# Performance work log

Measured on AMD Instinct MI355X. Metric: run time of the kernel, lower is better.

## Reference

```python
import jax, jax.numpy as jnp
import numpy as np
from jax import lax

E = 300      # _embsize
H = 32       # attention heads
ADIM = 64    # projection_dim (attention and values dim)
FF = 100     # feedforward hidden dim
NK = 11      # gaussian kernels
NCONV = 5    # conv kernel sizes 1..5
COUT = 16    # conv out channels for k>=2

def _kernel_mus(n):
    l = [1.0]
    b = 2.0 / (n - 1)
    l.append(1 - b / 2)
    for i in range(1, n - 1):
        l.append(l[i] - b)
    return l

def _kernel_sigmas(n):
    b = 2.0 / (n - 1)
    return [0.0001] + [0.5 * b] * (n - 1)

MU = jnp.asarray(_kernel_mus(NK), jnp.float32).reshape(1, 1, 1, 1, NK)
SIG = jnp.asarray(_kernel_sigmas(NK), jnp.float32).reshape(1, 1, 1, 1, NK)

def _pos_features(T, d):
    # allennlp add_positional_features, min_timescale=1, max_timescale=1e4, d even
    nt = d // 2
    inv = np.exp(np.arange(nt, dtype=np.float32) * -(np.log(1e4) / (nt - 1)))
    pos = np.arange(T, dtype=np.float32)[:, None] * inv[None, :]
    return jnp.asarray(np.concatenate([np.sin(pos), np.cos(pos)], axis=1))

def _layer_norm(x, g, b, eps=1e-6):
    m = jnp.mean(x, -1, keepdims=True)
    s = jnp.std(x, -1, keepdims=True)  # biased std, as allennlp LayerNorm
    return g * (x - m) / (s + eps) + b

def _mhsa(x, mask, Wc, bc, Wo, bo):
    # allennlp MultiHeadSelfAttention: combined projection, scale=sqrt(input_dim//heads)
    B, T, _ = x.shape
    comb = x @ Wc + bc                                   # [B,T,3*ADIM]
    q, k, v = comb[..., :ADIM], comb[..., ADIM:2 * ADIM], comb[..., 2 * ADIM:]
    dh = ADIM // H
    split = lambda t: t.reshape(B, T, H, dh).transpose(0, 2, 1, 3)
    q, k, v = split(q), split(k), split(v)
    scale = float(np.sqrt(E // H))
    sim = jnp.einsum('bhqd,bhkd->bhqk', q / scale, k)
    m = mask[:, None, None, :]
    p = jax.nn.softmax(sim * m, axis=-1) * m             # old allennlp masked_softmax
    p = p / (jnp.sum(p, -1, keepdims=True) + 1e-13)
    o = jnp.einsum('bhqk,bhkd->bhqd', p, v).transpose(0, 2, 1, 3).reshape(B, T, ADIM)
    return o @ Wo + bo

def _encode(x, mask, W1, b1, W2, b2, ffg, ffb, Wc, bc, Wo, bo, lng, lnb):
    # StackedSelfAttentionEncoder, 1 layer, all dropouts = 0
    out = x + _pos_features(x.shape[1], E)[None]
    ff = jax.nn.relu(out @ W1 + b1) @ W2 + b2
    ff = _layer_norm(ff + out, ffg, ffb)                 # residual (dims match)
    att = _mhsa(ff, mask, Wc, bc, Wo, bo)
    return _layer_norm(att + ff, lng, lnb)

def _conv(x, w, b, k):
    if k > 1:
        x = jnp.pad(x, ((0, 0), (0, 0), (0, k - 1), (0, k - 1)))  # ConstantPad2d(0,k-1,0,k-1)
    y = lax.conv_general_dilated(x, w, (1, 1), 'VALID',
                                 dimension_numbers=('NCHW', 'OIHW', 'NCHW'))
    y = y + b[None, :, None, None]
    if k > 1:
        y = jnp.max(y, axis=1, keepdims=True)            # MaxPool3d over channel dim
    return y

def setup_inputs() -> dict:
    key = jax.random.key(0)
    ks = iter(jax.random.split(key, 40))
    B, Q, D = 16, 32, 512
    nrm = lambda shape, s=0.05: jax.random.normal(next(ks), shape, jnp.float32) * s
    return {
        'query_embeddings': jax.random.normal(next(ks), (B, Q, E), jnp.float32),
        'document_embeddings': jax.random.normal(next(ks), (B, D, E), jnp.float32),
        'query_pad_oov_mask': jnp.ones((B, Q), jnp.float32),
        'document_pad_oov_mask': jnp.ones((B, D), jnp.float32),
        'query_idfs': jax.random.uniform(next(ks), (B, Q, 1), jnp.float32),
        'document_idfs': jax.random.uniform(next(ks), (B, D, 1), jnp.float32),
        'W1': nrm((E, FF)), 'b1': jnp.zeros((FF,), jnp.float32),
        'W2': nrm((FF, E)), 'b2': jnp.zeros((E,), jnp.float32),
        'ffg': jnp.ones((E,), jnp.float32), 'ffb': jnp.zeros((E,), jnp.float32),
        'Wc': nrm((E, 3 * ADIM)), 'bc': jnp.zeros((3 * ADIM,), jnp.float32),
        'Wo': nrm((ADIM, E)), 'bo': jnp.zeros((E,), jnp.float32),
        'lng': jnp.ones((E,), jnp.float32), 'lnb': jnp.zeros((E,), jnp.float32),
        'c1w': nrm((1, 2, 1, 1)), 'c1b': jnp.zeros((1,), jnp.float32),
        'c2w': nrm((COUT, 2, 2, 2)), 'c2b': jnp.zeros((COUT,), jnp.float32),
        'c3w': nrm((COUT, 2, 3, 3)), 'c3b': jnp.zeros((COUT,), jnp.float32),
        'c4w': nrm((COUT, 2, 4, 4)), 'c4b': jnp.zeros((COUT,), jnp.float32),
        'c5w': nrm((COUT, 2, 5, 5)), 'c5b': jnp.zeros((COUT,), jnp.float32),
        'dw': nrm((1, NK * NCONV)), 'db': jnp.zeros((1,), jnp.float32),
        'dmw': nrm((1, NK * NCONV)), 'dmb': jnp.zeros((1,), jnp.float32),
        'cw': nrm((1, 2)),
    }

def reference(query_embeddings, document_embeddings, query_pad_oov_mask,
              document_pad_oov_mask, query_idfs, document_idfs,
              W1, b1, W2, b2, ffg, ffb, Wc, bc, Wo, bo, lng, lnb,
              c1w, c1b, c2w, c2b, c3w, c3b, c4w, c4b, c5w, c5b,
              dw, db, dmw, dmb, cw):
    qm, dmask = query_pad_oov_mask, document_pad_oov_mask
    enc = lambda x, m: _encode(x, m, W1, b1, W2, b2, ffg, ffb, Wc, bc, Wo, bo, lng, lnb)
    q_ctx = enc(query_embeddings, qm) * qm[..., None]
    d_ctx = enc(document_embeddings, dmask) * dmask[..., None]
    # cosine on raw embeddings, dot product on contextualized
    qn = query_embeddings / (jnp.linalg.norm(query_embeddings, axis=-1, keepdims=True) + 1e-13)
    dn = document_embeddings / (jnp.linalg.norm(document_embeddings, axis=-1, keepdims=True) + 1e-13)
    cos = jnp.einsum('bqe,bde->bqd', qn, dn)[:, None]
    dot = jnp.einsum('bqe,bde->bqd', q_ctx, d_ctx)[:, None]
    combined = jnp.tanh(jnp.concatenate([cos, dot], axis=1))     # [B,2,Q,D]
    convs = [_conv(combined, w, b, k) for k, (w, b) in enumerate(
        [(c1w, c1b), (c2w, c2b), (c3w, c3b), (c4w, c4b), (c5w, c5b)], start=1)]
    all_conv = jnp.concatenate(convs, axis=1)[..., None]         # [B,5,Q,D,1]
    qd_mask = (qm[:, :, None] * dmask[:, None, :])[:, None, :, :, None]  # [B,1,Q,D,1]
    raw = jnp.exp(-(all_conv - MU) ** 2 / (2.0 * SIG ** 2))      # [B,5,Q,D,NK]
    masked = raw * qd_mask
    doc_len = jnp.sum(dmask, 1)                                  # [B]
    pkq = jnp.sum(masked, axis=3)                                # [B,5,Q,NK]
    log_pkq = jnp.log(jnp.clip(pkq, 1e-10, None)) * qm[:, None, :, None]
    per_kernel = jnp.sum(log_pkq, axis=2)                        # [B,5,NK]
    pkq_mean = pkq / doc_len[:, None, None, None]
    log_pkq_mean = jnp.log(jnp.clip(pkq_mean, 1e-10, None)) * qm[:, None, :, None]
    per_kernel_mean = jnp.sum(log_pkq_mean, axis=2)
    B = per_kernel.shape[0]
    d1 = per_kernel.reshape(B, -1) @ dw.T + db
    d2 = per_kernel_mean.reshape(B, -1) @ dmw.T + dmb
    return (jnp.concatenate([d1, d2], axis=1) @ cw.T)[:, 0]
```

## Files before the change

### kernel.cpp

```cpp
#include <hip/hip_runtime.h>

namespace {

constexpr int E_  = 300;
constexpr int FF_ = 100;
constexpr int AD_ = 64;
constexpr int NH_ = 32;
constexpr int CD_ = 192;
constexpr int B_  = 16;
constexpr int TQ_ = 32;
constexpr int TD_ = 512;
constexpr int NK_ = 11;
constexpr int DOCBLK_ = 512;

__device__ __forceinline__ float wave_sum(float v) {
#pragma unroll
  for (int o = 32; o > 0; o >>= 1) v += __shfl_down(v, o);
  return v;
}

__device__ __forceinline__ int swz16(int e, int t) {
  return e * 16 + (t ^ (((e >> 2) & 7) << 1));
}

__device__ __forceinline__ void fma4(float4& a, float s, const float4& w) {
  a.x = fmaf(s, w.x, a.x); a.y = fmaf(s, w.y, a.y);
  a.z = fmaf(s, w.z, a.z); a.w = fmaf(s, w.w, a.w);
}

__device__ __forceinline__ void gl_lds16(const float4* g, float4* l) {
  __builtin_amdgcn_global_load_lds(
      (const __attribute__((address_space(1))) void*)g,
      (__attribute__((address_space(3))) void*)l, 16, 0, 0);
}

__device__ __forceinline__ void stage_chunk(const float4* __restrict__ src,
                                            float4* __restrict__ dst,
                                            int n, int tid) {
  for (int j = tid; j < n; j += 256) gl_lds16(src + j, dst + j);
}

__global__ __launch_bounds__(256)
void encode_front_v5(const float* __restrict__ qe, const float* __restrict__ de,
                     const float* __restrict__ W1, const float* __restrict__ b1,
                     const float* __restrict__ W2, const float* __restrict__ b2,
                     const float* __restrict__ ffg, const float* __restrict__ ffb,
                     const float* __restrict__ Wc, const float* __restrict__ bc,
                     float* __restrict__ ffq, float* __restrict__ combq,
                     float* __restrict__ qn,
                     float* __restrict__ ffd, float* __restrict__ combd,
                     float* __restrict__ dnT)
{
  __shared__ float  s_A[4800];
  __shared__ float  s_h1[1600];
  __shared__ float4 s_w[2][1500];
  __shared__ float  s_stat[16][17];
  __shared__ float  s_norm[16];

  const int tid = threadIdx.x;
  const int ct = tid & 31, tg = tid >> 5;
  const int t0 = tg * 2;
  const bool doc = (blockIdx.x < DOCBLK_);
  const int sb = doc ? blockIdx.x : (blockIdx.x - DOCBLK_);
  const float* xs = (doc ? de : qe) + (size_t)sb * 16 * E_;
  float* ffo = doc ? ffd : ffq;
  float* cmo = doc ? combd : combq;
  const size_t tok0 = (size_t)sb * 16;
  const int bb_ = doc ? (int)(tok0 >> 9) : (int)(tok0 >> 5);
  const int tp0 = doc ? (int)(tok0 & 511) : (int)(tok0 & 31);

  const float4* W1f4 = (const float4*)W1;
  const float4* W2f4 = (const float4*)W2;
  const float4* Wcf4 = (const float4*)Wc;

  stage_chunk(W1f4, &s_w[0][0], 1500, tid);

  for (int i = tid; i < 1200; i += 256) {
    const float4 v = *(const float4*)(xs + (size_t)i * 4);
    const int t = i / 75, e0 = (i % 75) * 4;
    s_A[swz16(e0 + 0, t)] = v.x; s_A[swz16(e0 + 1, t)] = v.y;
    s_A[swz16(e0 + 2, t)] = v.z; s_A[swz16(e0 + 3, t)] = v.w;
  }
  __syncthreads();
  {
    const int tk = tid & 15, ch = tid >> 4;
    const int kb = ch * 19, ke = (kb + 19 < 300) ? kb + 19 : 300;
    float ss = 0.f;
    for (int k = kb; k < ke; ++k) { const float v = s_A[swz16(k, tk)]; ss = fmaf(v, v, ss); }
    s_stat[ch][tk] = ss;
  }
  __syncthreads();
  if (tid < 16) {
    float s = 0.f;
#pragma unroll
    for (int i = 0; i < 16; ++i) s += s_stat[i][tid];
    s_norm[tid] = 1.f / (sqrtf(s) + 1e-13f);
  }
  __syncthreads();
  for (int i = tid; i < 1200; i += 256) {
    const int t = i / 75, e0 = (i % 75) * 4;
    const int tp = tp0 + t;
    const float nm = s_norm[t];
#pragma unroll
    for (int j = 0; j < 4; ++j) {
      const int e = e0 + j;
      const int slot = swz16(e, t);
      const float raw = s_A[slot];
      if (doc) dnT[((size_t)bb_ * E_ + e) * 512 + tp] = raw * nm;
      else     qn[(tok0 + t) * E_ + e] = raw * nm;
      const int f = (e < 150) ? e : e - 150;
      const float ang = __expf(-0.061814365f * (float)f) * (float)tp;
      s_A[slot] = raw + ((e < 150) ? sinf(ang) : cosf(ang));
    }
  }
  __syncthreads();

  {
    const int cq = (ct < 25) ? ct : 24;
    float4 a1[2];
    a1[0] = make_float4(0.f, 0.f, 0.f, 0.f);
    a1[1] = make_float4(0.f, 0.f, 0.f, 0.f);
    for (int c = 0; c < 5; ++c) {
      if (c < 4) stage_chunk(W1f4 + 1500 * (c + 1), &s_w[(c + 1) & 1][0], 1500, tid);
      else       stage_chunk(W2f4,                  &s_w[1][0],           1500, tid);
      const float4* wb = &s_w[c & 1][0];
#pragma unroll 6
      for (int kk = 0; kk < 60; ++kk) {
        const float2 xv = *(const float2*)&s_A[swz16(c * 60 + kk, t0)];
        const float4 w = wb[kk * 25 + cq];
        fma4(a1[0], xv.x, w); fma4(a1[1], xv.y, w);
      }
      if (c == 4 && ct < 25) {
        const float4 bb = *(const float4*)&b1[4 * ct];
#pragma unroll
        for (int r = 0; r < 2; ++r) {
          const int t = t0 + r;
          const float4 a = (r == 0) ? a1[0] : a1[1];
          s_h1[swz16(4 * ct + 0, t)] = fmaxf(a.x + bb.x, 0.f);
          s_h1[swz16(4 * ct + 1, t)] = fmaxf(a.y + bb.y, 0.f);
          s_h1[swz16(4 * ct + 2, t)] = fmaxf(a.z + bb.z, 0.f);
          s_h1[swz16(4 * ct + 3, t)] = fmaxf(a.w + bb.w, 0.f);
        }
      }
      __syncthreads();
    }
  }

  {
    const int q2 = (ct < 11) ? ct + 64 : 74;
    const bool val2 = (ct < 11);
    float4 a2[3][2];
#pragma unroll
    for (int p = 0; p < 3; ++p)
#pragma unroll
      for (int r = 0; r < 2; ++r) a2[p][r] = make_float4(0.f, 0.f, 0.f, 0.f);
    for (int c = 0; c < 5; ++c) {
      if (c < 4) stage_chunk(W2f4 + 1500 * (c + 1), &s_w[c & 1][0], 1500, tid);
      else       stage_chunk(Wcf4,                  &s_w[0][0],     1440, tid);
      const float4* wb = &s_w[(c + 1) & 1][0];
#pragma unroll 5
      for (int kk = 0; kk < 20; ++kk) {
        const float2 hv = *(const float2*)&s_h1[swz16(c * 20 + kk, t0)];
        const float4 w0 = wb[kk * 75 + ct];
        const float4 w1 = wb[kk * 75 + ct + 32];
        const float4 w2 = wb[kk * 75 + q2];
        fma4(a2[0][0], hv.x, w0); fma4(a2[0][1], hv.y, w0);
        fma4(a2[1][0], hv.x, w1); fma4(a2[1][1], hv.y, w1);
        fma4(a2[2][0], hv.x, w2); fma4(a2[2][1], hv.y, w2);
      }
      if (c == 4) {
        float sum[2] = {0.f, 0.f}, sq[2] = {0.f, 0.f};
#pragma unroll
        for (int p = 0; p < 3; ++p) {
          const int qq = (p == 0) ? ct : (p == 1) ? ct + 32 : q2;
          const bool ok = (p < 2) || val2;
          if (!ok) break;
          const float4 bb = *(const float4*)&b2[4 * qq];
#pragma unroll
          for (int r = 0; r < 2; ++r) {
            const int t = t0 + r;
            float4 v = a2[p][r];
            v.x += bb.x + s_A[swz16(4 * qq + 0, t)];
            v.y += bb.y + s_A[swz16(4 * qq + 1, t)];
            v.z += bb.z + s_A[swz16(4 * qq + 2, t)];
            v.w += bb.w + s_A[swz16(4 * qq + 3, t)];
            a2[p][r] = v;
            sum[r] += v.x + v.y + v.z + v.w;
            sq[r] = fmaf(v.x, v.x, fmaf(v.y, v.y, fmaf(v.z, v.z, fmaf(v.w, v.w, sq[r]))));
          }
        }
#pragma unroll
        for (int m = 1; m <= 16; m <<= 1) {
#pragma unroll
          for (int r = 0; r < 2; ++r) {
            sum[r] += __shfl_xor(sum[r], m);
            sq[r]  += __shfl_xor(sq[r], m);
          }
        }
#pragma unroll
        for (int r = 0; r < 2; ++r) {
          const int t = t0 + r;
          const float mean = sum[r] * (1.f / 300.f);
          const float var  = fmaxf(sq[r] * (1.f / 300.f) - mean * mean, 0.f);
          const float rstd = 1.f / (sqrtf(var) + 1e-6f);
#pragma unroll
          for (int p = 0; p < 3; ++p) {
            if (p == 2 && !val2) break;
            const int qq = (p == 0) ? ct : (p == 1) ? ct + 32 : q2;
            const int c0 = 4 * qq;
            const float4 g4 = *(const float4*)&ffg[c0];
            const float4 b4 = *(const float4*)&ffb[c0];
            const float4 v = a2[p][r];
            float4 fv;
            fv.x = fmaf(g4.x, (v.x - mean) * rstd, b4.x);
            fv.y = fmaf(g4.y, (v.y - mean) * rstd, b4.y);
            fv.z = fmaf(g4.z, (v.z - mean) * rstd, b4.z);
            fv.w = fmaf(g4.w, (v.w - mean) * rstd, b4.w);
            *(float4*)&ffo[(tok0 + t) * E_ + c0] = fv;
            s_A[swz16(c0 + 0, t)] = fv.x; s_A[swz16(c0 + 1, t)] = fv.y;
            s_A[swz16(c0 + 2, t)] = fv.z; s_A[swz16(c0 + 3, t)] = fv.w;
          }
        }
      }
      __syncthreads();
    }
  }

  {
    const int q3 = (ct < 16) ? ct + 32 : 47;
    float4 a3[2][2];
#pragma unroll
    for (int p = 0; p < 2; ++p)
#pragma unroll
      for (int r = 0; r < 2; ++r) a3[p][r] = make_float4(0.f, 0.f, 0.f, 0.f);
    for (int c = 0; c < 10; ++c) {
      if (c < 9) stage_chunk(Wcf4 + 1440 * (c + 1), &s_w[(c + 1) & 1][0], 1440, tid);
      const float4* wb = &s_w[c & 1][0];
#pragma unroll 6
      for (int kk = 0; kk < 30; ++kk) {
        const float2 xv = *(const float2*)&s_A[swz16(c * 30 + kk, t0)];
        const float4 w0 = wb[kk * 48 + ct];
        const float4 w1 = wb[kk * 48 + q3];
        fma4(a3[0][0], xv.x, w0); fma4(a3[0][1], xv.y, w0);
        fma4(a3[1][0], xv.x, w1); fma4(a3[1][1], xv.y, w1);
      }
      if (c < 9) __syncthreads();
    }
    const float4 bb0 = *(const float4*)&bc[4 * ct];
#pragma unroll
    for (int r = 0; r < 2; ++r) {
      float4 o = a3[0][r];
      o.x += bb0.x; o.y += bb0.y; o.z += bb0.z; o.w += bb0.w;
      *(float4*)&cmo[(tok0 + t0 + r) * CD_ + 4 * ct] = o;
    }
    if (ct < 16) {
      const float4 bb1 = *(const float4*)&bc[4 * (ct + 32)];
#pragma unroll
      for (int r = 0; r < 2; ++r) {
        float4 o = a3[1][r];
        o.x += bb1.x; o.y += bb1.y; o.z += bb1.z; o.w += bb1.w;
        *(float4*)&cmo[(tok0 + t0 + r) * CD_ + 4 * (ct + 32)] = o;
      }
    }
  }
}

template <int T>
__global__ __launch_bounds__(512)
void attn(const float* __restrict__ comb, const float* __restrict__ mask,
          float* __restrict__ o)
{
  __shared__ float4 s_kv[T];
  __shared__ float  s_m[T];
  const int bh = blockIdx.x, b = bh / NH_, h = bh % NH_;
  const int tid = threadIdx.x;
  const float* cb = comb + (size_t)b * T * CD_;
  if (tid < T) {
    const float* c = cb + (size_t)tid * CD_;
    const float m = mask[b * T + tid];
    s_kv[tid] = make_float4(c[AD_ + 2 * h] * m, c[AD_ + 2 * h + 1] * m,
                            c[2 * AD_ + 2 * h], c[2 * AD_ + 2 * h + 1]);
    s_m[tid] = m;
  }
  __syncthreads();
  if (tid < T) {
    const float* c = cb + (size_t)tid * CD_;
    const float q0 = c[2 * h] * (1.f / 3.f);
    const float q1 = c[2 * h + 1] * (1.f / 3.f);
    float M = -1e30f;
    for (int j = 0; j < T; ++j) {
      const float4 kv = s_kv[j];
      M = fmaxf(M, fmaf(q0, kv.x, q1 * kv.y));
    }
    float S = 0.f, W = 0.f, a0 = 0.f, a1 = 0.f;
    for (int j = 0; j < T; ++j) {
      const float4 kv = s_kv[j];
      const float s = fmaf(q0, kv.x, q1 * kv.y);
      const float z = __expf(s - M);
      const float w = z * s_m[j];
      S += z; W += w;
      a0 = fmaf(w, kv.z, a0);
      a1 = fmaf(w, kv.w, a1);
    }
    const float dn = 1.f / (W + 1e-13f * S);
    float* op = o + (size_t)(b * T + tid) * AD_ + 2 * h;
    op[0] = a0 * dn;
    op[1] = a1 * dn;
  }
}

__global__ __launch_bounds__(256)
void encode_back_v3(const float* __restrict__ oq, const float* __restrict__ od,
                    const float* __restrict__ ffq, const float* __restrict__ ffd,
                    const float* __restrict__ Wo, const float* __restrict__ bo,
                    const float* __restrict__ lng, const float* __restrict__ lnb,
                    const float* __restrict__ qm, const float* __restrict__ dm,
                    float* __restrict__ qctx, float* __restrict__ dctxT)
{
  __shared__ float  s_O[1024];
  __shared__ float4 s_w[2][1200];

  const int tid = threadIdx.x;
  const int ct = tid & 31, tg = tid >> 5;
  const int t0 = tg * 2;
  const bool doc = (blockIdx.x < DOCBLK_);
  const int sb = doc ? blockIdx.x : (blockIdx.x - DOCBLK_);
  const size_t tok0 = (size_t)sb * 16;
  const float* op = doc ? od : oq;
  const float* ffp = doc ? ffd : ffq;
  const float* mp = doc ? dm : qm;
  const int bb_ = doc ? (int)(tok0 >> 9) : 0;
  const int tp0 = doc ? (int)(tok0 & 511) : 0;

  const float4* Wof4 = (const float4*)Wo;
  stage_chunk(Wof4, &s_w[0][0], 1200, tid);

  {
    const int t = tid >> 4, c0 = (tid & 15) * 4;
    const float4 v = *(const float4*)(op + (tok0 + t) * AD_ + c0);
    s_O[swz16(c0 + 0, t)] = v.x; s_O[swz16(c0 + 1, t)] = v.y;
    s_O[swz16(c0 + 2, t)] = v.z; s_O[swz16(c0 + 3, t)] = v.w;
  }
  __syncthreads();

  const int q2 = (ct < 11) ? ct + 64 : 74;
  const bool val2 = (ct < 11);
  float4 a[3][2];
#pragma unroll
  for (int p = 0; p < 3; ++p)
#pragma unroll
    for (int r = 0; r < 2; ++r) a[p][r] = make_float4(0.f, 0.f, 0.f, 0.f);
  for (int c = 0; c < 4; ++c) {
    if (c < 3) stage_chunk(Wof4 + 1200 * (c + 1), &s_w[(c + 1) & 1][0], 1200, tid);
    const float4* wb = &s_w[c & 1][0];
#pragma unroll 4
    for (int kk = 0; kk < 16; ++kk) {
      const float2 ov = *(const float2*)&s_O[swz16(c * 16 + kk, t0)];
      const float4 w0 = wb[kk * 75 + ct];
      const float4 w1 = wb[kk * 75 + ct + 32];
      const float4 w2 = wb[kk * 75 + q2];
      fma4(a[0][0], ov.x, w0); fma4(a[0][1], ov.y, w0);
      fma4(a[1][0], ov.x, w1); fma4(a[1][1], ov.y, w1);
      fma4(a[2][0], ov.x, w2); fma4(a[2][1], ov.y, w2);
    }
    if (c < 3) __syncthreads();
  }
  float sum[2] = {0.f, 0.f}, sq[2] = {0.f, 0.f};
#pragma unroll
  for (int p = 0; p < 3; ++p) {
    const int qq = (p == 0) ? ct : (p == 1) ? ct + 32 : q2;
    const bool ok = (p < 2) || val2;
    if (!ok) break;
    const float4 bb = *(const float4*)&bo[4 * qq];
#pragma unroll
    for (int r = 0; r < 2; ++r) {
      const int t = t0 + r;
      const float4 f4 = *(const float4*)(ffp + (tok0 + t) * E_ + 4 * qq);
      float4 v = a[p][r];
      v.x += bb.x + f4.x; v.y += bb.y + f4.y;
      v.z += bb.z + f4.z; v.w += bb.w + f4.w;
      a[p][r] = v;
      sum[r] += v.x + v.y + v.z + v.w;
      sq[r] = fmaf(v.x, v.x, fmaf(v.y, v.y, fmaf(v.z, v.z, fmaf(v.w, v.w, sq[r]))));
    }
  }
#pragma unroll
  for (int m = 1; m <= 16; m <<= 1) {
#pragma unroll
    for (int r = 0; r < 2; ++r) {
      sum[r] += __shfl_xor(sum[r], m);
      sq[r]  += __shfl_xor(sq[r], m);
    }
  }
#pragma unroll
  for (int r = 0; r < 2; ++r) {
    const int t = t0 + r;
    const float mean = sum[r] * (1.f / 300.f);
    const float var  = fmaxf(sq[r] * (1.f / 300.f) - mean * mean, 0.f);
    const float rstd = 1.f / (sqrtf(var) + 1e-6f);
    const float mk = mp[tok0 + t];
#pragma unroll
    for (int p = 0; p < 3; ++p) {
      if (p == 2 && !val2) break;
      const int qq = (p == 0) ? ct : (p == 1) ? ct + 32 : q2;
      const int c0 = 4 * qq;
      const float4 g4 = *(const float4*)&lng[c0];
      const float4 b4 = *(const float4*)&lnb[c0];
      const float4 v = a[p][r];
      float4 fv;
      fv.x = fmaf(g4.x, (v.x - mean) * rstd, b4.x) * mk;
      fv.y = fmaf(g4.y, (v.y - mean) * rstd, b4.y) * mk;
      fv.z = fmaf(g4.z, (v.z - mean) * rstd, b4.z) * mk;
      fv.w = fmaf(g4.w, (v.w - mean) * rstd, b4.w) * mk;
      if (doc) {
        const int tp = tp0 + t;
        dctxT[((size_t)bb_ * E_ + c0 + 0) * 512 + tp] = fv.x;
        dctxT[((size_t)bb_ * E_ + c0 + 1) * 512 + tp] = fv.y;
        dctxT[((size_t)bb_ * E_ + c0 + 2) * 512 + tp] = fv.z;
        dctxT[((size_t)bb_ * E_ + c0 + 3) * 512 + tp] = fv.w;
      } else {
        *(float4*)&qctx[(tok0 + t) * E_ + c0] = fv;
      }
    }
  }
}

__global__ __launch_bounds__(512)
void simtanh_v2(const float* __restrict__ qctx, const float* __restrict__ qn,
                const float* __restrict__ dctxT, const float* __restrict__ dnT,
                float* __restrict__ combined)
{
  __shared__ float s_q[2 * 16 * 304];
  __shared__ float s_part[8 * 32 * 64];

  const int bid = blockIdx.x;
  const int sub = bid & 15, b = bid >> 4;
  const int qh = sub >> 3, dc = sub & 7;
  const int tid = threadIdx.x;
  const int ep = tid >> 6, dlane = tid & 63;
  const int d = dc * 64 + dlane;

  const float* qc  = qctx + ((size_t)b * 32 + qh * 16) * E_;
  const float* qnp = qn   + ((size_t)b * 32 + qh * 16) * E_;
  for (int i = tid; i < 1200; i += 512) {
    const int q = i / 75, e0 = (i % 75) * 4;
    *(float4*)&s_q[(0 * 16 + q) * 304 + e0] = *(const float4*)(qc + q * E_ + e0);
    *(float4*)&s_q[(1 * 16 + q) * 304 + e0] = *(const float4*)(qnp + q * E_ + e0);
  }
  __syncthreads();

  const float* dct = dctxT + (size_t)b * E_ * 512 + d;
  const float* dnt = dnT   + (size_t)b * E_ * 512 + d;
  float accD[16], accC[16];
#pragma unroll
  for (int q = 0; q < 16; ++q) { accD[q] = 0.f; accC[q] = 0.f; }
  const int es = ep * 40, ee = (es + 40 < 300) ? es + 40 : 300;
  for (int e0 = es; e0 < ee; e0 += 4) {
    const float dv0 = dct[(size_t)(e0 + 0) * 512];
    const float dv1 = dct[(size_t)(e0 + 1) * 512];
    const float dv2 = dct[(size_t)(e0 + 2) * 512];
    const float dv3 = dct[(size_t)(e0 + 3) * 512];
    const float dn0 = dnt[(size_t)(e0 + 0) * 512];
    const float dn1 = dnt[(size_t)(e0 + 1) * 512];
    const float dn2 = dnt[(size_t)(e0 + 2) * 512];
    const float dn3 = dnt[(size_t)(e0 + 3) * 512];
#pragma unroll
    for (int q = 0; q < 16; ++q) {
      const float4 qd = *(const float4*)&s_q[(0 * 16 + q) * 304 + e0];
      const float4 qc4 = *(const float4*)&s_q[(1 * 16 + q) * 304 + e0];
      float aD = accD[q], aC = accC[q];
      aD = fmaf(qd.x, dv0, aD); aD = fmaf(qd.y, dv1, aD);
      aD = fmaf(qd.z, dv2, aD); aD = fmaf(qd.w, dv3, aD);
      aC = fmaf(qc4.x, dn0, aC); aC = fmaf(qc4.y, dn1, aC);
      aC = fmaf(qc4.z, dn2, aC); aC = fmaf(qc4.w, dn3, aC);
      accD[q] = aD; accC[q] = aC;
    }
  }
#pragma unroll
  for (int q = 0; q < 16; ++q) {
    s_part[(ep * 32 + q * 2 + 0) * 64 + dlane] = accC[q];
    s_part[(ep * 32 + q * 2 + 1) * 64 + dlane] = accD[q];
  }
  __syncthreads();
  const int s0 = (tid >> 6) * 4;
#pragma unroll
  for (int si = 0; si < 4; ++si) {
    const int s = s0 + si;
    float v = 0.f;
#pragma unroll
    for (int p = 0; p < 8; ++p) v += s_part[(p * 32 + s) * 64 + dlane];
    const int q = s >> 1, typ = s & 1;
    combined[(((size_t)b * 2 + typ) * 32 + qh * 16 + q) * 512 + d] = tanhf(v);
  }
}

template <int K>
__device__ __forceinline__ float conv_max16(const float* __restrict__ s_in, int j,
                                            const float* __restrict__ w,
                                            const float* __restrict__ bias)
{
  float patch[2][K][K];
#pragma unroll
  for (int c = 0; c < 2; ++c)
#pragma unroll
    for (int di = 0; di < K; ++di)
#pragma unroll
      for (int dj = 0; dj < K; ++dj)
        patch[c][di][dj] = s_in[(c * 5 + di) * 516 + j + dj];
  float best = -1e30f;
#pragma unroll
  for (int oc = 0; oc < 16; ++oc) {
    float acc = bias[oc];
#pragma unroll
    for (int c = 0; c < 2; ++c)
#pragma unroll
      for (int di = 0; di < K; ++di)
#pragma unroll
        for (int dj = 0; dj < K; ++dj)
          acc = fmaf(patch[c][di][dj], w[((oc * 2 + c) * K + di) * K + dj], acc);
    best = fmaxf(best, acc);
  }
  return best;
}

__global__ __launch_bounds__(512)
void conv_all(const float* __restrict__ combined,
              const float* __restrict__ c1w, const float* __restrict__ c1b,
              const float* __restrict__ c2w, const float* __restrict__ c2b,
              const float* __restrict__ c3w, const float* __restrict__ c3b,
              const float* __restrict__ c4w, const float* __restrict__ c4b,
              const float* __restrict__ c5w, const float* __restrict__ c5b,
              float* __restrict__ convout)
{
  __shared__ float s_in[2 * 5 * 516];
  __shared__ float s_w[1730];
  __shared__ float s_b[66];
  const int blk = blockIdx.x, b = blk >> 5, i = blk & 31;
  const int tid = threadIdx.x;
  for (int idx = tid; idx < 2 * 5 * 516; idx += 512) {
    const int c = idx / (5 * 516), rem = idx % (5 * 516), r = rem / 516, j = rem % 516;
    const int row = i + r;
    float v = 0.f;
    if (row < 32 && j < 512)
      v = combined[((size_t)(b * 2 + c) * 32 + row) * 512 + j];
    s_in[idx] = v;
  }
  if (tid < 2)   s_w[tid] = c1w[tid];
  if (tid < 128) s_w[2 + tid] = c2w[tid];
  if (tid < 288) s_w[130 + tid] = c3w[tid];
  s_w[418 + tid] = c4w[tid];
  for (int idx = tid; idx < 800; idx += 512) s_w[930 + idx] = c5w[idx];
  if (tid == 0) s_b[0] = c1b[0];
  if (tid < 16) {
    s_b[1 + tid]  = c2b[tid];
    s_b[17 + tid] = c3b[tid];
    s_b[33 + tid] = c4b[tid];
    s_b[49 + tid] = c5b[tid];
  }
  __syncthreads();
  const int j = tid;
  const float o1 = fmaf(s_in[j], s_w[0], fmaf(s_in[5 * 516 + j], s_w[1], s_b[0]));
  convout[((size_t)(b * 5 + 0) * 32 + i) * 512 + j] = o1;
  convout[((size_t)(b * 5 + 1) * 32 + i) * 512 + j] = conv_max16<2>(s_in, j, s_w + 2,   s_b + 1);
  convout[((size_t)(b * 5 + 2) * 32 + i) * 512 + j] = conv_max16<3>(s_in, j, s_w + 130, s_b + 17);
  convout[((size_t)(b * 5 + 3) * 32 + i) * 512 + j] = conv_max16<4>(s_in, j, s_w + 418, s_b + 33);
  convout[((size_t)(b * 5 + 4) * 32 + i) * 512 + j] = conv_max16<5>(s_in, j, s_w + 930, s_b + 49);
}

__global__ __launch_bounds__(512)
void rbf_pkq(const float* __restrict__ convout, const float* __restrict__ dmask,
             const float* __restrict__ qmask, float* __restrict__ pkq)
{
  __shared__ float red[8][NK_];
  const int id = blockIdx.x;
  const int q = id & 31;
  const int b = id / 160;
  const int tid = threadIdx.x;
  const float x = convout[(size_t)id * 512 + tid];
  const float dmv = dmask[b * 512 + tid];
  const float mu[NK_]  = {1.f, .9f, .7f, .5f, .3f, .1f, -.1f, -.3f, -.5f, -.7f, -.9f};
  const float nis[NK_] = {-5e7f, -50.f, -50.f, -50.f, -50.f, -50.f,
                          -50.f, -50.f, -50.f, -50.f, -50.f};
  const int lane = tid & 63, w = tid >> 6;
#pragma unroll
  for (int k = 0; k < NK_; ++k) {
    const float df = x - mu[k];
    float v = __expf(df * df * nis[k]) * dmv;
    v = wave_sum(v);
    if (lane == 0) red[w][k] = v;
  }
  __syncthreads();
  if (tid < NK_) {
    float s = 0.f;
#pragma unroll
    for (int ww = 0; ww < 8; ++ww) s += red[ww][tid];
    pkq[(size_t)id * NK_ + tid] = s * qmask[b * 32 + q];
  }
}

__global__ __launch_bounds__(64)
void final_k(const float* __restrict__ pkq, const float* __restrict__ qmask,
             const float* __restrict__ dmask,
             const float* __restrict__ dw, const float* __restrict__ db,
             const float* __restrict__ dmw, const float* __restrict__ dmb,
             const float* __restrict__ cw, float* __restrict__ out)
{
  const int b = blockIdx.x, tid = threadIdx.x;
  float dl = 0.f;
  for (int j = tid; j < 512; j += 64) dl += dmask[b * 512 + j];
  dl = wave_sum(dl);
  dl = __shfl(dl, 0);
  float v1 = 0.f, v2 = 0.f;
  if (tid < 55) {
    const int c = tid / NK_, k = tid % NK_;
    const float rdl = 1.f / dl;
    float s1 = 0.f, s2 = 0.f;
    for (int q = 0; q < 32; ++q) {
      const float p = pkq[(size_t)((b * 5 + c) * 32 + q) * NK_ + k];
      const float qmv = qmask[b * 32 + q];
      s1 += logf(fmaxf(p, 1e-10f)) * qmv;
      s2 += logf(fmaxf(p * rdl, 1e-10f)) * qmv;
    }
    v1 = s1 * dw[tid];
    v2 = s2 * dmw[tid];
  }
  v1 = wave_sum(v1);
  v2 = wave_sum(v2);
  if (tid == 0) out[b] = (v1 + db[0]) * cw[0] + (v2 + dmb[0]) * cw[1];
}

}

extern "C" void kernel_launch(void* const* d_in, const int* in_sizes, int n_in,
                              void* d_out, int out_size, void* d_ws, size_t ws_size,
                              hipStream_t stream)
{
  const float* qe  = (const float*)d_in[0];
  const float* de  = (const float*)d_in[1];
  const float* qm  = (const float*)d_in[2];
  const float* dm  = (const float*)d_in[3];
  const float* W1  = (const float*)d_in[6];
  const float* b1  = (const float*)d_in[7];
  const float* W2  = (const float*)d_in[8];
  const float* b2  = (const float*)d_in[9];
  const float* ffg = (const float*)d_in[10];
  const float* ffb = (const float*)d_in[11];
  const float* Wc  = (const float*)d_in[12];
  const float* bc  = (const float*)d_in[13];
  const float* Wo  = (const float*)d_in[14];
  const float* bo  = (const float*)d_in[15];
  const float* lng = (const float*)d_in[16];
  const float* lnb = (const float*)d_in[17];
  const float* c1w = (const float*)d_in[18];
  const float* c1b = (const float*)d_in[19];
  const float* c2w = (const float*)d_in[20];
  const float* c2b = (const float*)d_in[21];
  const float* c3w = (const float*)d_in[22];
  const float* c3b = (const float*)d_in[23];
  const float* c4w = (const float*)d_in[24];
  const float* c4b = (const float*)d_in[25];
  const float* c5w = (const float*)d_in[26];
  const float* c5b = (const float*)d_in[27];
  const float* dwp  = (const float*)d_in[28];
  const float* dbp  = (const float*)d_in[29];
  const float* dmwp = (const float*)d_in[30];
  const float* dmbp = (const float*)d_in[31];
  const float* cwp  = (const float*)d_in[32];

  float* ws = (float*)d_ws;
  size_t off = 0;
  auto alloc = [&](size_t n) { float* p = ws + off; off += n; return p; };
  float* ffq      = alloc((size_t)B_ * TQ_ * E_);
  float* combq    = alloc((size_t)B_ * TQ_ * CD_);
  float* oq       = alloc((size_t)B_ * TQ_ * AD_);
  float* qctx     = alloc((size_t)B_ * TQ_ * E_);
  float* qn       = alloc((size_t)B_ * TQ_ * E_);
  float* ffd      = alloc((size_t)B_ * TD_ * E_);
  float* combd    = alloc((size_t)B_ * TD_ * CD_);
  float* od       = alloc((size_t)B_ * TD_ * AD_);
  float* dctxT    = alloc((size_t)B_ * E_ * TD_);
  float* dnT      = alloc((size_t)B_ * E_ * TD_);
  float* combined = alloc((size_t)B_ * 2 * TQ_ * TD_);
  float* convout  = alloc((size_t)B_ * 5 * TQ_ * TD_);
  float* pkq      = alloc((size_t)B_ * 5 * TQ_ * NK_);

  encode_front_v5<<<DOCBLK_ + 32, 256, 0, stream>>>(
      qe, de, W1, b1, W2, b2, ffg, ffb, Wc, bc,
      ffq, combq, qn, ffd, combd, dnT);
  attn<TQ_><<<B_ * NH_, 64, 0, stream>>>(combq, qm, oq);
  attn<TD_><<<B_ * NH_, 512, 0, stream>>>(combd, dm, od);
  encode_back_v3<<<DOCBLK_ + 32, 256, 0, stream>>>(
      oq, od, ffq, ffd, Wo, bo, lng, lnb, qm, dm, qctx, dctxT);
  simtanh_v2<<<256, 512, 0, stream>>>(qctx, qn, dctxT, dnT, combined);
  conv_all<<<B_ * 32, 512, 0, stream>>>(
      combined, c1w, c1b, c2w, c2b, c3w, c3b, c4w, c4b, c5w, c5b, convout);
  rbf_pkq<<<B_ * 5 * TQ_, 512, 0, stream>>>(convout, dm, qm, pkq);
  final_k<<<B_, 64, 0, stream>>>(pkq, qm, dm, dwp, dbp, dmwp, dmbp, cwp,
                                 (float*)d_out);
}
```

Measured before the change: 382.0 us.

## Fuse conv and RBF pooling; stage weights via registers with single LDS buffer

The conv kernel now computes the gaussian kernel pooling directly on its five conv outputs. This removes the convout intermediate buffer (B*5*Q*D floats) and the separate rbf_pkq launch. Separately, the encoder kernels drop the async global_load_lds double buffer. They instead prefetch the next weight chunk into registers, commit it to a single LDS buffer and add a barrier per chunk, which halves weight LDS use but adds register pressure and extra synchronisation.

```diff
diff --git a/kernel.cpp b/kernel.cpp
--- a/kernel.cpp
+++ b/kernel.cpp
@@ -28,20 +28,8 @@
   a.z = fmaf(s, w.z, a.z); a.w = fmaf(s, w.w, a.w);
 }
 
-__device__ __forceinline__ void gl_lds16(const float4* g, float4* l) {
-  __builtin_amdgcn_global_load_lds(
-      (const __attribute__((address_space(1))) void*)g,
-      (__attribute__((address_space(3))) void*)l, 16, 0, 0);
-}
-
-__device__ __forceinline__ void stage_chunk(const float4* __restrict__ src,
-                                            float4* __restrict__ dst,
-                                            int n, int tid) {
-  for (int j = tid; j < n; j += 256) gl_lds16(src + j, dst + j);
-}
-
 __global__ __launch_bounds__(256)
-void encode_front_v5(const float* __restrict__ qe, const float* __restrict__ de,
+void encode_front_v8(const float* __restrict__ qe, const float* __restrict__ de,
                      const float* __restrict__ W1, const float* __restrict__ b1,
                      const float* __restrict__ W2, const float* __restrict__ b2,
                      const float* __restrict__ ffg, const float* __restrict__ ffb,
@@ -53,7 +41,7 @@
 {
   __shared__ float  s_A[4800];
   __shared__ float  s_h1[1600];
-  __shared__ float4 s_w[2][1500];
+  __shared__ float4 s_w4[1500];
   __shared__ float  s_stat[16][17];
   __shared__ float  s_norm[16];
 
@@ -73,7 +61,16 @@
   const float4* W2f4 = (const float4*)W2;
   const float4* Wcf4 = (const float4*)Wc;
 
-  stage_chunk(W1f4, &s_w[0][0], 1500, tid);
+  float4 r0, r1, r2, r3, r4, r5;
+#define LOADC(srcp, n) { const float4* _s = (srcp); \
+    r0 = _s[tid]; r1 = _s[tid + 256]; r2 = _s[tid + 512]; \
+    r3 = _s[tid + 768]; r4 = _s[tid + 1024]; \
+    if (tid + 1280 < (n)) r5 = _s[tid + 1280]; }
+#define COMMITC(n) { s_w4[tid] = r0; s_w4[tid + 256] = r1; s_w4[tid + 512] = r2; \
+    s_w4[tid + 768] = r3; s_w4[tid + 1024] = r4; \
+    if (tid + 1280 < (n)) s_w4[tid + 1280] = r5; }
+
+  LOADC(W1f4, 1500);
 
   for (int i = tid; i < 1200; i += 256) {
     const float4 v = *(const float4*)(xs + (size_t)i * 4);
@@ -121,21 +118,22 @@
     a1[0] = make_float4(0.f, 0.f, 0.f, 0.f);
     a1[1] = make_float4(0.f, 0.f, 0.f, 0.f);
     for (int c = 0; c < 5; ++c) {
-      if (c < 4) stage_chunk(W1f4 + 1500 * (c + 1), &s_w[(c + 1) & 1][0], 1500, tid);
-      else       stage_chunk(W2f4,                  &s_w[1][0],           1500, tid);
-      const float4* wb = &s_w[c & 1][0];
+      COMMITC(1500);
+      __syncthreads();
+      if (c < 4) LOADC(W1f4 + 1500 * (c + 1), 1500)
+      else       LOADC(W2f4, 1500)
 #pragma unroll 6
       for (int kk = 0; kk < 60; ++kk) {
         const float2 xv = *(const float2*)&s_A[swz16(c * 60 + kk, t0)];
-        const float4 w = wb[kk * 25 + cq];
+        const float4 w = s_w4[kk * 25 + cq];
         fma4(a1[0], xv.x, w); fma4(a1[1], xv.y, w);
       }
       if (c == 4 && ct < 25) {
         const float4 bb = *(const float4*)&b1[4 * ct];
 #pragma unroll
-        for (int r = 0; r < 2; ++r) {
-          const int t = t0 + r;
-          const float4 a = (r == 0) ? a1[0] : a1[1];
+        for (int rr = 0; rr < 2; ++rr) {
+          const int t = t0 + rr;
+          const float4 a = (rr == 0) ? a1[0] : a1[1];
           s_h1[swz16(4 * ct + 0, t)] = fmaxf(a.x + bb.x, 0.f);
           s_h1[swz16(4 * ct + 1, t)] = fmaxf(a.y + bb.y, 0.f);
           s_h1[swz16(4 * ct + 2, t)] = fmaxf(a.z + bb.z, 0.f);
@@ -153,17 +151,18 @@
 #pragma unroll
     for (int p = 0; p < 3; ++p)
 #pragma unroll
-      for (int r = 0; r < 2; ++r) a2[p][r] = make_float4(0.f, 0.f, 0.f, 0.f);
+      for (int rr = 0; rr < 2; ++rr) a2[p][rr] = make_float4(0.f, 0.f, 0.f, 0.f);
     for (int c = 0; c < 5; ++c) {
-      if (c < 4) stage_chunk(W2f4 + 1500 * (c + 1), &s_w[c & 1][0], 1500, tid);
-      else       stage_chunk(Wcf4,                  &s_w[0][0],     1440, tid);
-      const float4* wb = &s_w[(c + 1) & 1][0];
+      COMMITC(1500);
+      __syncthreads();
+      if (c < 4) LOADC(W2f4 + 1500 * (c + 1), 1500)
+      else       LOADC(Wcf4, 1440)
 #pragma unroll 5
       for (int kk = 0; kk < 20; ++kk) {
         const float2 hv = *(const float2*)&s_h1[swz16(c * 20 + kk, t0)];
-        const float4 w0 = wb[kk * 75 + ct];
-        const float4 w1 = wb[kk * 75 + ct + 32];
-        const float4 w2 = wb[kk * 75 + q2];
+        const float4 w0 = s_w4[kk * 75 + ct];
+        const float4 w1 = s_w4[kk * 75 + ct + 32];
+        const float4 w2 = s_w4[kk * 75 + q2];
         fma4(a2[0][0], hv.x, w0); fma4(a2[0][1], hv.y, w0);
         fma4(a2[1][0], hv.x, w1); fma4(a2[1][1], hv.y, w1);
         fma4(a2[2][0], hv.x, w2); fma4(a2[2][1], hv.y, w2);
@@ -177,31 +176,31 @@
           if (!ok) break;
           const float4 bb = *(const float4*)&b2[4 * qq];
 #pragma unroll
-          for (int r = 0; r < 2; ++r) {
-            const int t = t0 + r;
-            float4 v = a2[p][r];
+          for (int rr = 0; rr < 2; ++rr) {
+            const int t = t0 + rr;
+            float4 v = a2[p][rr];
             v.x += bb.x + s_A[swz16(4 * qq + 0, t)];
             v.y += bb.y + s_A[swz16(4 * qq + 1, t)];
             v.z += bb.z + s_A[swz16(4 * qq + 2, t)];
             v.w += bb.w + s_A[swz16(4 * qq + 3, t)];
-            a2[p][r] = v;
-            sum[r] += v.x + v.y + v.z + v.w;
-            sq[r] = fmaf(v.x, v.x, fmaf(v.y, v.y, fmaf(v.z, v.z, fmaf(v.w, v.w, sq[r]))));
+            a2[p][rr] = v;
+            sum[rr] += v.x + v.y + v.z + v.w;
+            sq[rr] = fmaf(v.x, v.x, fmaf(v.y, v.y, fmaf(v.z, v.z, fmaf(v.w, v.w, sq[rr]))));
           }
         }
 #pragma unroll
         for (int m = 1; m <= 16; m <<= 1) {
 #pragma unroll
-          for (int r = 0; r < 2; ++r) {
-            sum[r] += __shfl_xor(sum[r], m);
-            sq[r]  += __shfl_xor(sq[r], m);
+          for (int rr = 0; rr < 2; ++rr) {
+            sum[rr] += __shfl_xor(sum[rr], m);
+            sq[rr]  += __shfl_xor(sq[rr], m);
           }
         }
 #pragma unroll
-        for (int r = 0; r < 2; ++r) {
-          const int t = t0 + r;
-          const float mean = sum[r] * (1.f / 300.f);
-          const float var  = fmaxf(sq[r] * (1.f / 300.f) - mean * mean, 0.f);
+        for (int rr = 0; rr < 2; ++rr) {
+          const int t = t0 + rr;
+          const float mean = sum[rr] * (1.f / 300.f);
+          const float var  = fmaxf(sq[rr] * (1.f / 300.f) - mean * mean, 0.f);
           const float rstd = 1.f / (sqrtf(var) + 1e-6f);
 #pragma unroll
           for (int p = 0; p < 3; ++p) {
@@ -210,7 +209,7 @@
             const int c0 = 4 * qq;
             const float4 g4 = *(const float4*)&ffg[c0];
             const float4 b4 = *(const float4*)&ffb[c0];
-            const float4 v = a2[p][r];
+            const float4 v = a2[p][rr];
             float4 fv;
             fv.x = fmaf(g4.x, (v.x - mean) * rstd, b4.x);
             fv.y = fmaf(g4.y, (v.y - mean) * rstd, b4.y);
@@ -232,15 +231,16 @@
 #pragma unroll
     for (int p = 0; p < 2; ++p)
 #pragma unroll
-      for (int r = 0; r < 2; ++r) a3[p][r] = make_float4(0.f, 0.f, 0.f, 0.f);
+      for (int rr = 0; rr < 2; ++rr) a3[p][rr] = make_float4(0.f, 0.f, 0.f, 0.f);
     for (int c = 0; c < 10; ++c) {
-      if (c < 9) stage_chunk(Wcf4 + 1440 * (c + 1), &s_w[(c + 1) & 1][0], 1440, tid);
-      const float4* wb = &s_w[c & 1][0];
+      COMMITC(1440);
+      __syncthreads();
+      if (c < 9) LOADC(Wcf4 + 1440 * (c + 1), 1440)
 #pragma unroll 6
       for (int kk = 0; kk < 30; ++kk) {
         const float2 xv = *(const float2*)&s_A[swz16(c * 30 + kk, t0)];
-        const float4 w0 = wb[kk * 48 + ct];
-        const float4 w1 = wb[kk * 48 + q3];
+        const float4 w0 = s_w4[kk * 48 + ct];
+        const float4 w1 = s_w4[kk * 48 + q3];
         fma4(a3[0][0], xv.x, w0); fma4(a3[0][1], xv.y, w0);
         fma4(a3[1][0], xv.x, w1); fma4(a3[1][1], xv.y, w1);
       }
@@ -248,21 +248,23 @@
     }
     const float4 bb0 = *(const float4*)&bc[4 * ct];
 #pragma unroll
-    for (int r = 0; r < 2; ++r) {
-      float4 o = a3[0][r];
+    for (int rr = 0; rr < 2; ++rr) {
+      float4 o = a3[0][rr];
       o.x += bb0.x; o.y += bb0.y; o.z += bb0.z; o.w += bb0.w;
-      *(float4*)&cmo[(tok0 + t0 + r) * CD_ + 4 * ct] = o;
+      *(float4*)&cmo[(tok0 + t0 + rr) * CD_ + 4 * ct] = o;
     }
     if (ct < 16) {
       const float4 bb1 = *(const float4*)&bc[4 * (ct + 32)];
 #pragma unroll
-      for (int r = 0; r < 2; ++r) {
-        float4 o = a3[1][r];
+      for (int rr = 0; rr < 2; ++rr) {
+        float4 o = a3[1][rr];
         o.x += bb1.x; o.y += bb1.y; o.z += bb1.z; o.w += bb1.w;
-        *(float4*)&cmo[(tok0 + t0 + r) * CD_ + 4 * (ct + 32)] = o;
+        *(float4*)&cmo[(tok0 + t0 + rr) * CD_ + 4 * (ct + 32)] = o;
       }
     }
   }
+#undef LOADC
+#undef COMMITC
 }
 
 template <int T>
@@ -310,7 +312,7 @@
 }
 
 __global__ __launch_bounds__(256)
-void encode_back_v3(const float* __restrict__ oq, const float* __restrict__ od,
+void encode_back_v8(const float* __restrict__ oq, const float* __restrict__ od,
                     const float* __restrict__ ffq, const float* __restrict__ ffd,
                     const float* __restrict__ Wo, const float* __restrict__ bo,
                     const float* __restrict__ lng, const float* __restrict__ lnb,
@@ -318,7 +320,7 @@
                     float* __restrict__ qctx, float* __restrict__ dctxT)
 {
   __shared__ float  s_O[1024];
-  __shared__ float4 s_w[2][1200];
+  __shared__ float4 s_wb[1200];
 
   const int tid = threadIdx.x;
   const int ct = tid & 31, tg = tid >> 5;
@@ -333,7 +335,15 @@
   const int tp0 = doc ? (int)(tok0 & 511) : 0;
 
   const float4* Wof4 = (const float4*)Wo;
-  stage_chunk(Wof4, &s_w[0][0], 1200, tid);
+
+  float4 r0, r1, r2, r3, r4;
+#define LOADB(srcp) { const float4* _s = (srcp); \
+    r0 = _s[tid]; r1 = _s[tid + 256]; r2 = _s[tid + 512]; r3 = _s[tid + 768]; \
+    if (tid + 1024 < 1200) r4 = _s[tid + 1024]; }
+#define COMMITB() { s_wb[tid] = r0; s_wb[tid + 256] = r1; s_wb[tid + 512] = r2; \
+    s_wb[tid + 768] = r3; if (tid + 1024 < 1200) s_wb[tid + 1024] = r4; }
+
+  LOADB(Wof4);
 
   {
     const int t = tid >> 4, c0 = (tid & 15) * 4;
@@ -349,16 +359,17 @@
 #pragma unroll
   for (int p = 0; p < 3; ++p)
 #pragma unroll
-    for (int r = 0; r < 2; ++r) a[p][r] = make_float4(0.f, 0.f, 0.f, 0.f);
+    for (int rr = 0; rr < 2; ++rr) a[p][rr] = make_float4(0.f, 0.f, 0.f, 0.f);
   for (int c = 0; c < 4; ++c) {
-    if (c < 3) stage_chunk(Wof4 + 1200 * (c + 1), &s_w[(c + 1) & 1][0], 1200, tid);
-    const float4* wb = &s_w[c & 1][0];
+    COMMITB();
+    __syncthreads();
+    if (c < 3) LOADB(Wof4 + 1200 * (c + 1))
 #pragma unroll 4
     for (int kk = 0; kk < 16; ++kk) {
       const float2 ov = *(const float2*)&s_O[swz16(c * 16 + kk, t0)];
-      const float4 w0 = wb[kk * 75 + ct];
-      const float4 w1 = wb[kk * 75 + ct + 32];
-      const float4 w2 = wb[kk * 75 + q2];
+      const float4 w0 = s_wb[kk * 75 + ct];
+      const float4 w1 = s_wb[kk * 75 + ct + 32];
+      const float4 w2 = s_wb[kk * 75 + q2];
       fma4(a[0][0], ov.x, w0); fma4(a[0][1], ov.y, w0);
       fma4(a[1][0], ov.x, w1); fma4(a[1][1], ov.y, w1);
       fma4(a[2][0], ov.x, w2); fma4(a[2][1], ov.y, w2);
@@ -373,30 +384,30 @@
     if (!ok) break;
     const float4 bb = *(const float4*)&bo[4 * qq];
 #pragma unroll
-    for (int r = 0; r < 2; ++r) {
-      const int t = t0 + r;
+    for (int rr = 0; rr < 2; ++rr) {
+      const int t = t0 + rr;
       const float4 f4 = *(const float4*)(ffp + (tok0 + t) * E_ + 4 * qq);
-      float4 v = a[p][r];
+      float4 v = a[p][rr];
       v.x += bb.x + f4.x; v.y += bb.y + f4.y;
       v.z += bb.z + f4.z; v.w += bb.w + f4.w;
-      a[p][r] = v;
-      sum[r] += v.x + v.y + v.z + v.w;
-      sq[r] = fmaf(v.x, v.x, fmaf(v.y, v.y, fmaf(v.z, v.z, fmaf(v.w, v.w, sq[r]))));
+      a[p][rr] = v;
+      sum[rr] += v.x + v.y + v.z + v.w;
+      sq[rr] = fmaf(v.x, v.x, fmaf(v.y, v.y, fmaf(v.z, v.z, fmaf(v.w, v.w, sq[rr]))));
     }
   }
 #pragma unroll
   for (int m = 1; m <= 16; m <<= 1) {
 #pragma unroll
-    for (int r = 0; r < 2; ++r) {
-      sum[r] += __shfl_xor(sum[r], m);
-      sq[r]  += __shfl_xor(sq[r], m);
-    }
-  }
-#pragma unroll
-  for (int r = 0; r < 2; ++r) {
-    const int t = t0 + r;
-    const float mean = sum[r] * (1.f / 300.f);
-    const float var  = fmaxf(sq[r] * (1.f / 300.f) - mean * mean, 0.f);
+    for (int rr = 0; rr < 2; ++rr) {
+      sum[rr] += __shfl_xor(sum[rr], m);
+      sq[rr]  += __shfl_xor(sq[rr], m);
+    }
+  }
+#pragma unroll
+  for (int rr = 0; rr < 2; ++rr) {
+    const int t = t0 + rr;
+    const float mean = sum[rr] * (1.f / 300.f);
+    const float var  = fmaxf(sq[rr] * (1.f / 300.f) - mean * mean, 0.f);
     const float rstd = 1.f / (sqrtf(var) + 1e-6f);
     const float mk = mp[tok0 + t];
 #pragma unroll
@@ -406,7 +417,7 @@
       const int c0 = 4 * qq;
       const float4 g4 = *(const float4*)&lng[c0];
       const float4 b4 = *(const float4*)&lnb[c0];
-      const float4 v = a[p][r];
+      const float4 v = a[p][rr];
       float4 fv;
       fv.x = fmaf(g4.x, (v.x - mean) * rstd, b4.x) * mk;
       fv.y = fmaf(g4.y, (v.y - mean) * rstd, b4.y) * mk;
@@ -423,6 +434,8 @@
       }
     }
   }
+#undef LOADB
+#undef COMMITB
 }
 
 __global__ __launch_bounds__(512)
@@ -524,17 +537,19 @@
 }
 
 __global__ __launch_bounds__(512)
-void conv_all(const float* __restrict__ combined,
+void conv_rbf(const float* __restrict__ combined,
               const float* __restrict__ c1w, const float* __restrict__ c1b,
               const float* __restrict__ c2w, const float* __restrict__ c2b,
               const float* __restrict__ c3w, const float* __restrict__ c3b,
               const float* __restrict__ c4w, const float* __restrict__ c4b,
               const float* __restrict__ c5w, const float* __restrict__ c5b,
-              float* __restrict__ convout)
+              const float* __restrict__ dmask, const float* __restrict__ qmask,
+              float* __restrict__ pkq)
 {
   __shared__ float s_in[2 * 5 * 516];
   __shared__ float s_w[1730];
   __shared__ float s_b[66];
+  __shared__ float s_red[8][56];
   const int blk = blockIdx.x, b = blk >> 5, i = blk & 31;
   const int tid = threadIdx.x;
   for (int idx = tid; idx < 2 * 5 * 516; idx += 512) {
@@ -559,42 +574,35 @@
   }
   __syncthreads();
   const int j = tid;
-  const float o1 = fmaf(s_in[j], s_w[0], fmaf(s_in[5 * 516 + j], s_w[1], s_b[0]));
-  convout[((size_t)(b * 5 + 0) * 32 + i) * 512 + j] = o1;
-  convout[((size_t)(b * 5 + 1) * 32 + i) * 512 + j] = conv_max16<2>(s_in, j, s_w + 2,   s_b + 1);
-  convout[((size_t)(b * 5 + 2) * 32 + i) * 512 + j] = conv_max16<3>(s_in, j, s_w + 130, s_b + 17);
-  convout[((size_t)(b * 5 + 3) * 32 + i) * 512 + j] = conv_max16<4>(s_in, j, s_w + 418, s_b + 33);
-  convout[((size_t)(b * 5 + 4) * 32 + i) * 512 + j] = conv_max16<5>(s_in, j, s_w + 930, s_b + 49);
-}
-
-__global__ __launch_bounds__(512)
-void rbf_pkq(const float* __restrict__ convout, const float* __restrict__ dmask,
-             const float* __restrict__ qmask, float* __restrict__ pkq)
-{
-  __shared__ float red[8][NK_];
-  const int id = blockIdx.x;
-  const int q = id & 31;
-  const int b = id / 160;
-  const int tid = threadIdx.x;
-  const float x = convout[(size_t)id * 512 + tid];
-  const float dmv = dmask[b * 512 + tid];
+  float val[5];
+  val[0] = fmaf(s_in[j], s_w[0], fmaf(s_in[5 * 516 + j], s_w[1], s_b[0]));
+  val[1] = conv_max16<2>(s_in, j, s_w + 2,   s_b + 1);
+  val[2] = conv_max16<3>(s_in, j, s_w + 130, s_b + 17);
+  val[3] = conv_max16<4>(s_in, j, s_w + 418, s_b + 33);
+  val[4] = conv_max16<5>(s_in, j, s_w + 930, s_b + 49);
+
+  const float dmv = dmask[b * 512 + j];
   const float mu[NK_]  = {1.f, .9f, .7f, .5f, .3f, .1f, -.1f, -.3f, -.5f, -.7f, -.9f};
   const float nis[NK_] = {-5e7f, -50.f, -50.f, -50.f, -50.f, -50.f,
                           -50.f, -50.f, -50.f, -50.f, -50.f};
   const int lane = tid & 63, w = tid >> 6;
 #pragma unroll
-  for (int k = 0; k < NK_; ++k) {
-    const float df = x - mu[k];
-    float v = __expf(df * df * nis[k]) * dmv;
-    v = wave_sum(v);
-    if (lane == 0) red[w][k] = v;
-  }
-  __syncthreads();
-  if (tid < NK_) {
+  for (int c = 0; c < 5; ++c) {
+#pragma unroll
+    for (int k = 0; k < NK_; ++k) {
+      const float df = val[c] - mu[k];
+      float v = __expf(df * df * nis[k]) * dmv;
+      v = wave_sum(v);
+      if (lane == 0) s_red[w][c * NK_ + k] = v;
+    }
+  }
+  __syncthreads();
+  if (tid < 55) {
     float s = 0.f;
 #pragma unroll
-    for (int ww = 0; ww < 8; ++ww) s += red[ww][tid];
-    pkq[(size_t)id * NK_ + tid] = s * qmask[b * 32 + q];
+    for (int ww = 0; ww < 8; ++ww) s += s_red[ww][tid];
+    const int c = tid / NK_, k = tid % NK_;
+    pkq[((size_t)(b * 5 + c) * 32 + i) * NK_ + k] = s * qmask[b * 32 + i];
   }
 }
 
@@ -681,20 +689,19 @@
   float* dctxT    = alloc((size_t)B_ * E_ * TD_);
   float* dnT      = alloc((size_t)B_ * E_ * TD_);
   float* combined = alloc((size_t)B_ * 2 * TQ_ * TD_);
-  float* convout  = alloc((size_t)B_ * 5 * TQ_ * TD_);
   float* pkq      = alloc((size_t)B_ * 5 * TQ_ * NK_);
 
-  encode_front_v5<<<DOCBLK_ + 32, 256, 0, stream>>>(
+  encode_front_v8<<<DOCBLK_ + 32, 256, 0, stream>>>(
       qe, de, W1, b1, W2, b2, ffg, ffb, Wc, bc,
       ffq, combq, qn, ffd, combd, dnT);
   attn<TQ_><<<B_ * NH_, 64, 0, stream>>>(combq, qm, oq);
   attn<TD_><<<B_ * NH_, 512, 0, stream>>>(combd, dm, od);
-  encode_back_v3<<<DOCBLK_ + 32, 256, 0, stream>>>(
+  encode_back_v8<<<DOCBLK_ + 32, 256, 0, stream>>>(
       oq, od, ffq, ffd, Wo, bo, lng, lnb, qm, dm, qctx, dctxT);
   simtanh_v2<<<256, 512, 0, stream>>>(qctx, qn, dctxT, dnT, combined);
-  conv_all<<<B_ * 32, 512, 0, stream>>>(
-      combined, c1w, c1b, c2w, c2b, c3w, c3b, c4w, c4b, c5w, c5b, convout);
-  rbf_pkq<<<B_ * 5 * TQ_, 512, 0, stream>>>(convout, dm, qm, pkq);
+  conv_rbf<<<B_ * 32, 512, 0, stream>>>(
+      combined, c1w, c1b, c2w, c2b, c3w, c3b, c4w, c4b, c5w, c5b,
+      dm, qm, pkq);
   final_k<<<B_, 64, 0, stream>>>(pkq, qm, dm, dwp, dbp, dmwp, dmbp, cwp,
                                  (float*)d_out);
 }
```

After: 1.186 ms. 3.11x slower.
